# Performance work log

Hardware: AMD Instinct MI355X
Metric: run time of the kernel (lower is better)

## Reference

```python
import jax, jax.numpy as jnp
import numpy as np

B, C, H, W = 4, 64, 64, 64

def setup_inputs() -> dict:
    key = jax.random.key(0)
    ks = jax.random.split(key, 8)
    s = 1.0 / np.sqrt(C)
    return {
        "x": jax.random.normal(ks[0], (B, C, H, W), dtype=jnp.float32),
        "Wq": jax.random.normal(ks[1], (C, C), dtype=jnp.float32) * s,
        "bq": jax.random.normal(ks[2], (C,), dtype=jnp.float32) * s,
        "Wk": jax.random.normal(ks[3], (C, C), dtype=jnp.float32) * s,
        "bk": jax.random.normal(ks[4], (C,), dtype=jnp.float32) * s,
        "Wv": jax.random.normal(ks[5], (C, C), dtype=jnp.float32) * s,
        "bv": jax.random.normal(ks[6], (C,), dtype=jnp.float32) * s,
        "gamma": jax.random.normal(ks[7], (1,), dtype=jnp.float32),
    }

def reference(x, Wq, bq, Wk, bk, Wv, bv, gamma):
    b, c, h, w = x.shape
    xf = x.reshape(b, c, h * w)                      # [B, C, N]
    q = jnp.einsum('oc,bcn->bon', Wq, xf) + bq[None, :, None]
    k = jnp.einsum('oc,bcn->bon', Wk, xf) + bk[None, :, None]
    v = jnp.einsum('oc,bcn->bon', Wv, xf) + bv[None, :, None]
    energy = jnp.einsum('bci,bcj->bij', q, k)        # [B, N, N] = Q^T K
    attn = jax.nn.softmax(energy, axis=-1)
    # out[b,c,i] = sum_j v[b,c,j] * attn[b,i,j]
    out = jnp.einsum('bcj,bij->bci', v, attn)        # [B, C, N]
    out = out.reshape(b, c, h, w)
    return gamma[0] * out + x
```

## Files before the change

kernel.cpp:

```cpp
#include <hip/hip_runtime.h>
#include <hip/hip_bf16.h>
#include <math.h>


constexpr int C_ = 64;
constexpr int N_ = 4096;
constexpr float LOG2E = 1.4426950408889634f;
constexpr float MBIAS = 86.5617f;

typedef float  f4 __attribute__((ext_vector_type(4)));
typedef short  s8 __attribute__((ext_vector_type(8)));

__device__ inline unsigned short f2bf(float x) {
    union { float f; unsigned u; } a; a.f = x;
    unsigned r = a.u + 0x7FFFu + ((a.u >> 16) & 1u);
    return (unsigned short)(r >> 16);
}
__device__ inline float bf2f(unsigned short h) {
    union { float f; unsigned u; } a; a.u = ((unsigned)h) << 16; return a.f;
}
__device__ inline uint4 pack8(const float* v) {
    uint4 r;
    r.x = (unsigned)f2bf(v[0]) | ((unsigned)f2bf(v[1]) << 16);
    r.y = (unsigned)f2bf(v[2]) | ((unsigned)f2bf(v[3]) << 16);
    r.z = (unsigned)f2bf(v[4]) | ((unsigned)f2bf(v[5]) << 16);
    r.w = (unsigned)f2bf(v[6]) | ((unsigned)f2bf(v[7]) << 16);
    return r;
}
__device__ inline void pack8_split(const float* v, uint4* hi, uint4* lo) {
    unsigned short h[8]; float rem[8];
    #pragma unroll
    for (int i = 0; i < 8; ++i) { h[i] = f2bf(v[i]); rem[i] = v[i] - bf2f(h[i]); }
    hi->x = (unsigned)h[0] | ((unsigned)h[1] << 16);
    hi->y = (unsigned)h[2] | ((unsigned)h[3] << 16);
    hi->z = (unsigned)h[4] | ((unsigned)h[5] << 16);
    hi->w = (unsigned)h[6] | ((unsigned)h[7] << 16);
    *lo = pack8(rem);
}

__global__ __launch_bounds__(256) void prep_kernel(
    const float* __restrict__ x,
    const float* __restrict__ Wq, const float* __restrict__ bq,
    const float* __restrict__ Wk, const float* __restrict__ bk,
    const float* __restrict__ Wv, const float* __restrict__ bv,
    unsigned short* __restrict__ qhi, unsigned short* __restrict__ qlo,
    unsigned short* __restrict__ khi, unsigned short* __restrict__ klo,
    unsigned short* __restrict__ vv)
{
    __shared__ __align__(16) char smem[62208];
    float (*xs)[36]  = (float(*)[36])(smem);
    float (*wqs)[68] = (float(*)[68])(smem + 9216);
    float (*wks)[68] = (float(*)[68])(smem + 26624);
    float (*wvs)[68] = (float(*)[68])(smem + 44032);
    float* bias      = (float*)(smem + 61440);

    const int t    = threadIdx.x;
    const int nt2  = blockIdx.x, b = blockIdx.y;
    const int n0   = nt2 * 32;
    const int nt64 = nt2 >> 1, joff = (nt2 & 1) * 32;

    {
        const int nl = t & 31, cb = t >> 5;
        #pragma unroll
        for (int it = 0; it < 8; ++it) {
            int c = it * 8 + cb;
            xs[c][nl] = x[((long)b * 64 + c) * N_ + n0 + nl];
        }
        #pragma unroll
        for (int kk = 0; kk < 4; ++kk) {
            int f = t * 4 + kk * 1024;
            int o = f >> 6, c = f & 63;
            float4 w = *(const float4*)&Wq[f];
            wqs[c+0][o] = w.x; wqs[c+1][o] = w.y; wqs[c+2][o] = w.z; wqs[c+3][o] = w.w;
            w = *(const float4*)&Wk[f];
            wks[c+0][o] = w.x; wks[c+1][o] = w.y; wks[c+2][o] = w.z; wks[c+3][o] = w.w;
            w = *(const float4*)&Wv[f];
            wvs[c+0][o] = w.x; wvs[c+1][o] = w.y; wvs[c+2][o] = w.z; wvs[c+3][o] = w.w;
        }
        if (t < 64) { bias[t] = bq[t]; bias[64 + t] = bk[t]; bias[128 + t] = bv[t]; }
    }
    __syncthreads();

    const int o4 = (t & 15) * 4, n2 = (t >> 4) * 2;
    float aq[4][2], ak[4][2], av[4][2];
    #pragma unroll
    for (int oo = 0; oo < 4; ++oo) {
        aq[oo][0] = bias[o4 + oo];        aq[oo][1] = aq[oo][0];
        ak[oo][0] = bias[64 + o4 + oo];   ak[oo][1] = ak[oo][0];
        av[oo][0] = bias[128 + o4 + oo];  av[oo][1] = av[oo][0];
    }
    #pragma unroll 4
    for (int c = 0; c < 64; ++c) {
        float2 xv = *(const float2*)&xs[c][n2];
        f4 w1 = *(const f4*)&wqs[c][o4];
        f4 w2 = *(const f4*)&wks[c][o4];
        f4 w3 = *(const f4*)&wvs[c][o4];
        #pragma unroll
        for (int oo = 0; oo < 4; ++oo) {
            aq[oo][0] = fmaf(w1[oo], xv.x, aq[oo][0]);
            aq[oo][1] = fmaf(w1[oo], xv.y, aq[oo][1]);
            ak[oo][0] = fmaf(w2[oo], xv.x, ak[oo][0]);
            ak[oo][1] = fmaf(w2[oo], xv.y, ak[oo][1]);
            av[oo][0] = fmaf(w3[oo], xv.x, av[oo][0]);
            av[oo][1] = fmaf(w3[oo], xv.y, av[oo][1]);
        }
    }
    __syncthreads();

    {
        float (*qst)[68] = wqs;
        float (*kst)[68] = wks;
        float (*vst)[36] = xs;
        #pragma unroll
        for (int oo = 0; oo < 4; ++oo) {
            qst[n2][o4 + oo]     = aq[oo][0] * LOG2E;
            qst[n2 + 1][o4 + oo] = aq[oo][1] * LOG2E;
            kst[n2][o4 + oo]     = ak[oo][0];
            kst[n2 + 1][o4 + oo] = ak[oo][1];
            vst[o4 + oo][n2]     = av[oo][0];
            vst[o4 + oo][n2 + 1] = av[oo][1];
        }
    }
    __syncthreads();

    const long gbase = ((long)b * 64 + nt64) * 512;
    float tmp[8];
    {
        float (*qst)[68] = wqs;
        int mloc = t >> 7, ks = (t >> 6) & 1, L = t & 63;
        int m = (joff >> 4) + mloc;
        int rowl = mloc * 16 + (L & 15), c0 = ks * 32 + ((L >> 4) & 3) * 8;
        *(f4*)tmp       = *(const f4*)&qst[rowl][c0];
        *(f4*)(tmp + 4) = *(const f4*)&qst[rowl][c0 + 4];
        uint4 hi, lo; pack8_split(tmp, &hi, &lo);
        long ch = gbase + (m * 2 + ks) * 64 + L;
        *(uint4*)(qhi + ch * 8) = hi;
        *(uint4*)(qlo + ch * 8) = lo;
    }
    {
        float (*kst)[68] = wks;
        int cc = t >> 5, jl = t & 31;
        *(f4*)tmp       = *(const f4*)&kst[jl][cc * 8];
        *(f4*)(tmp + 4) = *(const f4*)&kst[jl][cc * 8 + 4];
        uint4 hi, lo; pack8_split(tmp, &hi, &lo);
        long ch = gbase + cc * 64 + joff + jl;
        *(uint4*)(khi + ch * 8) = hi;
        *(uint4*)(klo + ch * 8) = lo;
    }
    {
        float (*vst)[36] = xs;
        int cj = t >> 6, c = t & 63;
        *(f4*)tmp       = *(const f4*)&vst[c][cj * 8];
        *(f4*)(tmp + 4) = *(const f4*)&vst[c][cj * 8 + 4];
        long ch = gbase + ((joff >> 3) + cj) * 64 + c;
        *(uint4*)(vv + ch * 8) = pack8(tmp);
    }
}

__global__ __launch_bounds__(256, 4) void attn_kernel(
    const unsigned short* __restrict__ qhi, const unsigned short* __restrict__ qlo,
    const unsigned short* __restrict__ khi, const unsigned short* __restrict__ klo,
    const unsigned short* __restrict__ vv,
    unsigned* __restrict__ Opart, float* __restrict__ lpart,
    int njt, int Bn)
{
    __shared__ __align__(16) char pst_all[4 * 4608];

    const int t  = threadIdx.x;
    const int w  = t >> 6, L = t & 63;
    char* pst = pst_all + w * 4608;
    const int lh = L >> 4, ll = L & 15;
    const int ib2 = blockIdx.x * 4 + w;
    const int ib  = ib2 >> 1, mo = (ib2 & 1) * 2;
    const int jc = blockIdx.y, b = blockIdx.z;

    s8 qh[2][2], ql[2][2];
    {
        const int qb = (b * 64 + ib) * 512;
        #pragma unroll
        for (int m = 0; m < 2; ++m)
            #pragma unroll
            for (int ks = 0; ks < 2; ++ks) {
                int ch = qb + ((mo + m) * 2 + ks) * 64 + L;
                qh[m][ks] = *(const s8*)(qhi + (long)ch * 8);
                ql[m][ks] = *(const s8*)(qlo + (long)ch * 8);
            }
    }

    f4 O[2][4];
    #pragma unroll
    for (int m = 0; m < 2; ++m)
        #pragma unroll
        for (int nn = 0; nn < 4; ++nn) O[m][nn] = (f4){0.f, 0.f, 0.f, 0.f};
    float lp[2][4];
    #pragma unroll
    for (int m = 0; m < 2; ++m)
        #pragma unroll
        for (int r = 0; r < 4; ++r) lp[m][r] = 0.f;

    const int jt0 = jc * njt;
    for (int jt = 0; jt < njt; ++jt) {
        const int kb = (b * 64 + jt0 + jt) * 512;

        #pragma unroll
        for (int js = 0; js < 4; ++js) {
            __builtin_amdgcn_sched_barrier(0);
            s8 bh[2], bl[2];
            #pragma unroll
            for (int ks = 0; ks < 2; ++ks) {
                int ch = kb + (ks * 4 + lh) * 64 + js * 16 + ll;
                bh[ks] = *(const s8*)(khi + (long)ch * 8);
                bl[ks] = *(const s8*)(klo + (long)ch * 8);
            }
            #pragma unroll
            for (int m = 0; m < 2; ++m) {
                f4 acc = (f4){0.f, 0.f, 0.f, 0.f};
                acc = __builtin_amdgcn_mfma_f32_16x16x32_bf16(qh[m][0], bh[0], acc, 0, 0, 0);
                acc = __builtin_amdgcn_mfma_f32_16x16x32_bf16(qh[m][1], bh[1], acc, 0, 0, 0);
                acc = __builtin_amdgcn_mfma_f32_16x16x32_bf16(qh[m][0], bl[0], acc, 0, 0, 0);
                acc = __builtin_amdgcn_mfma_f32_16x16x32_bf16(qh[m][1], bl[1], acc, 0, 0, 0);
                acc = __builtin_amdgcn_mfma_f32_16x16x32_bf16(ql[m][0], bh[0], acc, 0, 0, 0);
                acc = __builtin_amdgcn_mfma_f32_16x16x32_bf16(ql[m][1], bh[1], acc, 0, 0, 0);
                #pragma unroll
                for (int r = 0; r < 4; ++r) {
                    float p = __builtin_amdgcn_exp2f(acc[r] - MBIAS);
                    lp[m][r] += p;
                    int row = m * 16 + lh * 4 + r;
                    int col = js * 16 + ll;
                    *(unsigned short*)(pst + row * 144 + col * 2) = f2bf(p);
                }
            }
        }
        __builtin_amdgcn_sched_barrier(0);

        #pragma unroll
        for (int ks = 0; ks < 2; ++ks) {
            s8 bvf[4];
            #pragma unroll
            for (int nn = 0; nn < 4; ++nn) {
                int ch = kb + (ks * 4 + lh) * 64 + nn * 16 + ll;
                bvf[nn] = *(const s8*)(vv + (long)ch * 8);
            }
            #pragma unroll
            for (int m = 0; m < 2; ++m) {
                s8 ap = *(const s8*)(pst + (m * 16 + ll) * 144 + ks * 64 + lh * 16);
                #pragma unroll
                for (int nn = 0; nn < 4; ++nn)
                    O[m][nn] = __builtin_amdgcn_mfma_f32_16x16x32_bf16(ap, bvf[nn], O[m][nn], 0, 0, 0);
            }
        }
    }

    #pragma unroll
    for (int m = 0; m < 2; ++m)
        #pragma unroll
        for (int r = 0; r < 4; ++r) {
            float s = lp[m][r];
            s += __shfl_xor(s, 1); s += __shfl_xor(s, 2);
            s += __shfl_xor(s, 4); s += __shfl_xor(s, 8);
            lp[m][r] = s;
        }
    const long obase = ((long)jc * Bn + b) * 128 + ib2;
    if (ll == 0) {
        #pragma unroll
        for (int m = 0; m < 2; ++m)
            #pragma unroll
            for (int r = 0; r < 4; ++r)
                lpart[obase * 32 + m * 16 + lh * 4 + r] = lp[m][r];
    }
    unsigned* op = Opart + obase * 1024;
    #pragma unroll
    for (int m = 0; m < 2; ++m)
        #pragma unroll
        for (int nn = 0; nn < 4; ++nn)
            #pragma unroll
            for (int rh = 0; rh < 2; ++rh) {
                unsigned lo = f2bf(O[m][nn][rh * 2]);
                unsigned hi = f2bf(O[m][nn][rh * 2 + 1]);
                op[((((m * 4 + nn) * 2) + rh) << 6) + L] = lo | (hi << 16);
            }
}

__global__ __launch_bounds__(512) void combine_kernel(
    const unsigned* __restrict__ Opart, const float* __restrict__ lpart,
    const float* __restrict__ x, const float* __restrict__ gamma_p,
    float* __restrict__ out, int js, int Bn)
{
    __shared__ float trn[64][36];
    __shared__ float lsc[32];
    const int t   = threadIdx.x;
    const int ib2 = blockIdx.x, b = blockIdx.y;
    const float g = gamma_p[0];

    float s[4] = {0.f, 0.f, 0.f, 0.f};
    for (int jc = 0; jc < js; ++jc) {
        const unsigned* base = Opart + (((long)jc * Bn + b) * 128 + ib2) * 1024;
        unsigned u0 = base[t];
        unsigned u1 = base[t + 512];
        s[0] += bf2f((unsigned short)(u0 & 0xffff));
        s[1] += bf2f((unsigned short)(u0 >> 16));
        s[2] += bf2f((unsigned short)(u1 & 0xffff));
        s[3] += bf2f((unsigned short)(u1 >> 16));
    }
    if (t < 32) {
        float ls = 0.f;
        for (int jc = 0; jc < js; ++jc)
            ls += lpart[(((long)jc * Bn + b) * 128 + ib2) * 32 + t];
        lsc[t] = g / ls;
    }
    #pragma unroll
    for (int e = 0; e < 2; ++e) {
        int u_idx = t + e * 512;
        int idx2 = u_idx >> 6, L = u_idx & 63;
        int m = idx2 >> 3, nn = (idx2 >> 1) & 3, rh = idx2 & 1;
        int col = nn * 16 + (L & 15);
        int row0 = m * 16 + (L >> 4) * 4 + rh * 2;
        trn[col][row0]     = s[e * 2 + 0];
        trn[col][row0 + 1] = s[e * 2 + 1];
    }
    __syncthreads();

    const int cl = t >> 3, nq = (t & 7) * 4;
    const long ob = ((long)b * 64 + cl) * N_ + ib2 * 32 + nq;
    float4 xr = *(const float4*)&x[ob];
    float4 rr;
    rr.x = trn[cl][nq + 0] * lsc[nq + 0] + xr.x;
    rr.y = trn[cl][nq + 1] * lsc[nq + 1] + xr.y;
    rr.z = trn[cl][nq + 2] * lsc[nq + 2] + xr.z;
    rr.w = trn[cl][nq + 3] * lsc[nq + 3] + xr.w;
    *(float4*)&out[ob] = rr;
}

extern "C" void kernel_launch(void* const* d_in, const int* in_sizes, int n_in,
                              void* d_out, int out_size, void* d_ws, size_t ws_size,
                              hipStream_t stream) {
    const float* x  = (const float*)d_in[0];
    const float* Wq = (const float*)d_in[1];
    const float* bq = (const float*)d_in[2];
    const float* Wk = (const float*)d_in[3];
    const float* bk = (const float*)d_in[4];
    const float* Wv = (const float*)d_in[5];
    const float* bv = (const float*)d_in[6];
    const float* gm = (const float*)d_in[7];
    float* out = (float*)d_out;

    const int B = in_sizes[0] / (C_ * N_);
    const size_t per = (size_t)B * N_ * C_;
    char* w = (char*)d_ws;
    unsigned short* qhi = (unsigned short*)w;
    unsigned short* qlo = qhi + per;
    unsigned short* khi = qlo + per;
    unsigned short* klo = khi + per;
    unsigned short* vv  = klo + per;
    size_t base = 5 * per * sizeof(unsigned short);

    int js = 16;
    while (js > 1) {
        size_t need = base + (size_t)js *
            ((size_t)B * 128 * 1024 * 4  + (size_t)B * 128 * 32 * 4 );
        if (need <= ws_size) break;
        js >>= 1;
    }
    unsigned* Opart = (unsigned*)(w + base);
    float* lpart = (float*)(w + base + (size_t)js * (size_t)B * 128 * 1024 * 4);

    prep_kernel<<<dim3(128, B), 256, 0, stream>>>(x, Wq, bq, Wk, bk, Wv, bv,
                                                  qhi, qlo, khi, klo, vv);
    attn_kernel<<<dim3(32, js, B), 256, 0, stream>>>(qhi, qlo, khi, klo, vv,
                                                     Opart, lpart, 64 / js, B);
    combine_kernel<<<dim3(128, B), 512, 0, stream>>>(Opart, lpart, x, gm, out, js, B);
}
```

Before: 137.4 us.

## Fuse split-K combine into attention kernel via last-block atomic ticket

Removes the separate combine kernel. Each attention block atomically increments a per-tile counter, and the last block to finish for a query tile reduces the partial outputs and writes the final result with gamma and the residual. The prep kernel resets the counters. The key split also drops from 16 to 8, which halves the partial-buffer traffic but gives the attention grid less parallelism. The final reduction is now serialized in one block per tile, and correctness depends on threadfence ordering.

```diff
diff --git a/kernel.cpp b/kernel.cpp
--- a/kernel.cpp
+++ b/kernel.cpp
@@ -45,7 +45,7 @@
     const float* __restrict__ Wv, const float* __restrict__ bv,
     unsigned short* __restrict__ qhi, unsigned short* __restrict__ qlo,
     unsigned short* __restrict__ khi, unsigned short* __restrict__ klo,
-    unsigned short* __restrict__ vv)
+    unsigned short* __restrict__ vv, unsigned* __restrict__ cnt)
 {
     __shared__ __align__(16) char smem[62208];
     float (*xs)[36]  = (float(*)[36])(smem);
@@ -58,6 +58,8 @@
     const int nt2  = blockIdx.x, b = blockIdx.y;
     const int n0   = nt2 * 32;
     const int nt64 = nt2 >> 1, joff = (nt2 & 1) * 32;
+
+    if (nt2 == 0 && t < 32) cnt[b * 32 + t] = 0;
 
     {
         const int nl = t & 31, cb = t >> 5;
@@ -160,17 +162,21 @@
 __global__ __launch_bounds__(256, 4) void attn_kernel(
     const unsigned short* __restrict__ qhi, const unsigned short* __restrict__ qlo,
     const unsigned short* __restrict__ khi, const unsigned short* __restrict__ klo,
-    const unsigned short* __restrict__ vv,
+    const unsigned short* __restrict__ vv, const float* __restrict__ x,
+    const float* __restrict__ gamma_p,
     unsigned* __restrict__ Opart, float* __restrict__ lpart,
-    int njt, int Bn)
+    unsigned* __restrict__ cnt, float* __restrict__ out,
+    int njt, int jsn, int Bn)
 {
     __shared__ __align__(16) char pst_all[4 * 4608];
+    __shared__ int ticket_s;
 
     const int t  = threadIdx.x;
     const int w  = t >> 6, L = t & 63;
     char* pst = pst_all + w * 4608;
     const int lh = L >> 4, ll = L & 15;
-    const int ib2 = blockIdx.x * 4 + w;
+    const int bx = blockIdx.x;
+    const int ib2 = bx * 4 + w;
     const int ib  = ib2 >> 1, mo = (ib2 & 1) * 2;
     const int jc = blockIdx.y, b = blockIdx.z;
 
@@ -279,56 +285,63 @@
                 unsigned hi = f2bf(O[m][nn][rh * 2 + 1]);
                 op[((((m * 4 + nn) * 2) + rh) << 6) + L] = lo | (hi << 16);
             }
-}
-
-__global__ __launch_bounds__(512) void combine_kernel(
-    const unsigned* __restrict__ Opart, const float* __restrict__ lpart,
-    const float* __restrict__ x, const float* __restrict__ gamma_p,
-    float* __restrict__ out, int js, int Bn)
-{
-    __shared__ float trn[64][36];
-    __shared__ float lsc[32];
-    const int t   = threadIdx.x;
-    const int ib2 = blockIdx.x, b = blockIdx.y;
+
+    __threadfence();
+    __syncthreads();
+    if (t == 0) ticket_s = (int)atomicAdd(&cnt[b * 32 + bx], 1u);
+    __syncthreads();
+    if (ticket_s != jsn - 1) return;
+    __threadfence();
+
+    float (*trn)[36] = (float(*)[36])pst_all;
+    float* lsc = (float*)(pst_all + 9216);
     const float g = gamma_p[0];
 
-    float s[4] = {0.f, 0.f, 0.f, 0.f};
-    for (int jc = 0; jc < js; ++jc) {
-        const unsigned* base = Opart + (((long)jc * Bn + b) * 128 + ib2) * 1024;
-        unsigned u0 = base[t];
-        unsigned u1 = base[t + 512];
-        s[0] += bf2f((unsigned short)(u0 & 0xffff));
-        s[1] += bf2f((unsigned short)(u0 >> 16));
-        s[2] += bf2f((unsigned short)(u1 & 0xffff));
-        s[3] += bf2f((unsigned short)(u1 >> 16));
-    }
-    if (t < 32) {
-        float ls = 0.f;
-        for (int jc = 0; jc < js; ++jc)
-            ls += lpart[(((long)jc * Bn + b) * 128 + ib2) * 32 + t];
-        lsc[t] = g / ls;
-    }
-    #pragma unroll
-    for (int e = 0; e < 2; ++e) {
-        int u_idx = t + e * 512;
-        int idx2 = u_idx >> 6, L = u_idx & 63;
-        int m = idx2 >> 3, nn = (idx2 >> 1) & 3, rh = idx2 & 1;
-        int col = nn * 16 + (L & 15);
-        int row0 = m * 16 + (L >> 4) * 4 + rh * 2;
-        trn[col][row0]     = s[e * 2 + 0];
-        trn[col][row0 + 1] = s[e * 2 + 1];
-    }
-    __syncthreads();
-
-    const int cl = t >> 3, nq = (t & 7) * 4;
-    const long ob = ((long)b * 64 + cl) * N_ + ib2 * 32 + nq;
-    float4 xr = *(const float4*)&x[ob];
-    float4 rr;
-    rr.x = trn[cl][nq + 0] * lsc[nq + 0] + xr.x;
-    rr.y = trn[cl][nq + 1] * lsc[nq + 1] + xr.y;
-    rr.z = trn[cl][nq + 2] * lsc[nq + 2] + xr.z;
-    rr.w = trn[cl][nq + 3] * lsc[nq + 3] + xr.w;
-    *(float4*)&out[ob] = rr;
+    for (int sl = 0; sl < 4; ++sl) {
+        const int ib2s = bx * 4 + sl;
+        float s[4][2];
+        #pragma unroll
+        for (int e = 0; e < 4; ++e) { s[e][0] = 0.f; s[e][1] = 0.f; }
+        for (int jc2 = 0; jc2 < jsn; ++jc2) {
+            const unsigned* base = Opart + (((long)jc2 * Bn + b) * 128 + ib2s) * 1024;
+            #pragma unroll
+            for (int e = 0; e < 4; ++e) {
+                unsigned u = base[t + e * 256];
+                s[e][0] += bf2f((unsigned short)(u & 0xffff));
+                s[e][1] += bf2f((unsigned short)(u >> 16));
+            }
+        }
+        __syncthreads();
+        if (t < 32) {
+            float ls = 0.f;
+            for (int jc2 = 0; jc2 < jsn; ++jc2)
+                ls += lpart[(((long)jc2 * Bn + b) * 128 + ib2s) * 32 + t];
+            lsc[t] = g / ls;
+        }
+        #pragma unroll
+        for (int e = 0; e < 4; ++e) {
+            int u_idx = t + e * 256;
+            int idx2 = u_idx >> 6, L2 = u_idx & 63;
+            int m = idx2 >> 3, nn = (idx2 >> 1) & 3, rh = idx2 & 1;
+            int col = nn * 16 + (L2 & 15);
+            int row0 = m * 16 + (L2 >> 4) * 4 + rh * 2;
+            trn[col][row0]     = s[e][0];
+            trn[col][row0 + 1] = s[e][1];
+        }
+        __syncthreads();
+        const int cl = t >> 2, nq = (t & 3) * 8;
+        const long ob = ((long)b * 64 + cl) * N_ + ib2s * 32 + nq;
+        #pragma unroll
+        for (int h = 0; h < 2; ++h) {
+            float4 xr = *(const float4*)&x[ob + h * 4];
+            float4 rr;
+            rr.x = trn[cl][nq + h*4 + 0] * lsc[nq + h*4 + 0] + xr.x;
+            rr.y = trn[cl][nq + h*4 + 1] * lsc[nq + h*4 + 1] + xr.y;
+            rr.z = trn[cl][nq + h*4 + 2] * lsc[nq + h*4 + 2] + xr.z;
+            rr.w = trn[cl][nq + h*4 + 3] * lsc[nq + h*4 + 3] + xr.w;
+            *(float4*)&out[ob + h * 4] = rr;
+        }
+    }
 }
 
 extern "C" void kernel_launch(void* const* d_in, const int* in_sizes, int n_in,
@@ -354,19 +367,20 @@
     unsigned short* vv  = klo + per;
     size_t base = 5 * per * sizeof(unsigned short);
 
-    int js = 16;
+    int js = 8;
     while (js > 1) {
         size_t need = base + (size_t)js *
-            ((size_t)B * 128 * 1024 * 4  + (size_t)B * 128 * 32 * 4 );
+            ((size_t)B * 128 * 1024 * 4 + (size_t)B * 128 * 32 * 4) + (size_t)B * 32 * 4;
         if (need <= ws_size) break;
         js >>= 1;
     }
     unsigned* Opart = (unsigned*)(w + base);
-    float* lpart = (float*)(w + base + (size_t)js * (size_t)B * 128 * 1024 * 4);
+    size_t lpoff = base + (size_t)js * (size_t)B * 128 * 1024 * 4;
+    float* lpart = (float*)(w + lpoff);
+    unsigned* cnt = (unsigned*)(w + lpoff + (size_t)js * (size_t)B * 128 * 32 * 4);
 
     prep_kernel<<<dim3(128, B), 256, 0, stream>>>(x, Wq, bq, Wk, bk, Wv, bv,
-                                                  qhi, qlo, khi, klo, vv);
-    attn_kernel<<<dim3(32, js, B), 256, 0, stream>>>(qhi, qlo, khi, klo, vv,
-                                                     Opart, lpart, 64 / js, B);
-    combine_kernel<<<dim3(128, B), 512, 0, stream>>>(Opart, lpart, x, gm, out, js, B);
-}
+                                                  qhi, qlo, khi, klo, vv, cnt);
+    attn_kernel<<<dim3(32, js, B), 256, 0, stream>>>(qhi, qlo, khi, klo, vv, x, gm,
+                                                     Opart, lpart, cnt, out, 64 / js, js, B);
+}
```

Measured after the change: 277.3 us. 102% more time.
